# Kernel optimization log

Measured on AMD Instinct MI355X. Metric: run time of the kernel, lower is better.

## Reference

```python
import jax, jax.numpy as jnp
import numpy as np

T, B, F_IN = 1024, 256, 87


def _lstm(x, Wih, Whh, b):
    """PyTorch-convention LSTM over seq-first x [T,B,In]; gate order i,f,g,o."""
    H = Whh.shape[1]
    Bz = x.shape[1]

    def step(carry, xt):
        h, c = carry
        z = xt @ Wih.T + h @ Whh.T + b  # [B, 4H]
        i, f, g, o = jnp.split(z, 4, axis=-1)
        c = jax.nn.sigmoid(f) * c + jax.nn.sigmoid(i) * jnp.tanh(g)
        h = jax.nn.sigmoid(o) * jnp.tanh(c)
        return (h, c), h

    init = (jnp.zeros((Bz, H), x.dtype), jnp.zeros((Bz, H), x.dtype))
    _, ys = jax.lax.scan(step, init, x)
    return ys  # [T, B, H]


def setup_inputs() -> dict:
    key = jax.random.key(0)
    ks = jax.random.split(key, 24)

    def p(k, shape, fan):
        s = 1.0 / np.sqrt(fan)
        return jax.random.uniform(k, shape, jnp.float32, -s, s)

    d = {}
    d["x"] = jax.random.normal(ks[0], (T, B, F_IN), jnp.float32)
    # LSTM params (bias = b_ih + b_hh combined; forward-equivalent)
    dims = [(F_IN, 256), (256, 128), (128, 64), (64, 32)]
    ki = 1
    for li, (din, h) in enumerate(dims, start=1):
        d[f"w{li}i"] = p(ks[ki], (4 * h, din), h); ki += 1
        d[f"w{li}h"] = p(ks[ki], (4 * h, h), h); ki += 1
        d[f"b{li}"] = p(ks[ki], (4 * h,), h); ki += 1
    fcs = [(32, 128), (128, 64), (64, 32), (32, 3)]
    for fi, (din, dout) in enumerate(fcs, start=1):
        d[f"f{fi}w"] = p(ks[ki], (dout, din), din); ki += 1
        d[f"f{fi}b"] = p(ks[ki], (dout,), din); ki += 1
    return d


def reference(x, w1i, w1h, b1, w2i, w2h, b2, w3i, w3h, b3, w4i, w4h, b4,
              f1w, f1b, f2w, f2b, f3w, f3b, f4w, f4b):
    h = jnp.tanh(_lstm(x, w1i, w1h, b1))
    h = jnp.tanh(_lstm(h, w2i, w2h, b2))
    h = jnp.tanh(_lstm(h, w3i, w3h, b3))
    h = jnp.tanh(_lstm(h, w4i, w4h, b4)[0])  # [0] -> first timestep, [B,32]
    h = jax.nn.relu(h @ f1w.T + f1b)
    h = jax.nn.relu(h @ f2w.T + f2b)
    h = jax.nn.relu(h @ f3w.T + f3b)
    return h @ f4w.T + f4b  # [B, 3]
```

## Files before the change

### kernel.cpp

```cpp
#include <hip/hip_runtime.h>
#include <math.h>


#define O_W1T 0
#define O_W2T 66816
#define O_W3T 165120
#define O_W4T 189696
#define O_F1T 195840
#define O_F2T 199936
#define O_F3T 208128
#define O_B1  210176
#define O_B2  210944
#define O_B3  211328
#define O_B4  211520

__global__ __launch_bounds__(256) void prep_kernel(
    const float* __restrict__ w1i, const float* __restrict__ w2i,
    const float* __restrict__ w3i, const float* __restrict__ w4i,
    const float* __restrict__ b1,  const float* __restrict__ b2,
    const float* __restrict__ b3,  const float* __restrict__ b4,
    const float* __restrict__ f1w, const float* __restrict__ f2w,
    const float* __restrict__ f3w, float* __restrict__ ws)
{
    int i = blockIdx.x * 256 + threadIdx.x;
    if (i < 89088) {
        int row = i / 87, k = i - row * 87;
        int g = row >> 8;
        if (g != 1) {
            int base = (g == 0) ? 0 : (g == 2) ? 256 : 512;
            ws[O_W1T + k * 768 + base + (row & 255)] = w1i[i];
        }
    } else if (i < 220160) {
        int l = i - 89088;
        int row = l >> 8, k = l & 255;
        int g = row >> 7;
        if (g != 1) {
            int base = (g == 0) ? 0 : (g == 2) ? 128 : 256;
            ws[O_W2T + k * 384 + base + (row & 127)] = w2i[l];
        }
    } else if (i < 252928) {
        int l = i - 220160;
        int row = l >> 7, k = l & 127;
        int g = row >> 6;
        if (g != 1) {
            int base = (g == 0) ? 0 : (g == 2) ? 64 : 128;
            ws[O_W3T + k * 192 + base + (row & 63)] = w3i[l];
        }
    } else if (i < 261120) {
        int l = i - 252928;
        int row = l >> 6, k = l & 63;
        int g = row >> 5;
        if (g != 1) {
            int base = (g == 0) ? 0 : (g == 2) ? 32 : 64;
            ws[O_W4T + k * 96 + base + (row & 31)] = w4i[l];
        }
    } else if (i < 262144) {
        int l = i - 261120;
        int g = l >> 8;
        if (g != 1) {
            int base = (g == 0) ? 0 : (g == 2) ? 256 : 512;
            ws[O_B1 + base + (l & 255)] = b1[l];
        }
    } else if (i < 262656) {
        int l = i - 262144;
        int g = l >> 7;
        if (g != 1) {
            int base = (g == 0) ? 0 : (g == 2) ? 128 : 256;
            ws[O_B2 + base + (l & 127)] = b2[l];
        }
    } else if (i < 262912) {
        int l = i - 262656;
        int g = l >> 6;
        if (g != 1) {
            int base = (g == 0) ? 0 : (g == 2) ? 64 : 128;
            ws[O_B3 + base + (l & 63)] = b3[l];
        }
    } else if (i < 263040) {
        int l = i - 262912;
        int g = l >> 5;
        if (g != 1) {
            int base = (g == 0) ? 0 : (g == 2) ? 32 : 64;
            ws[O_B4 + base + (l & 31)] = b4[l];
        }
    } else if (i < 267136) {
        int l = i - 263040;
        int j = l >> 5, k = l & 31;
        ws[O_F1T + k * 128 + j] = f1w[l];
    } else if (i < 275328) {
        int l = i - 267136;
        int j = l >> 7, k = l & 127;
        ws[O_F2T + k * 64 + j] = f2w[l];
    } else if (i < 277376) {
        int l = i - 275328;
        int j = l >> 6, k = l & 63;
        ws[O_F3T + k * 32 + j] = f3w[l];
    }
}

__device__ __forceinline__ float frcp(float x) { return __builtin_amdgcn_rcpf(x); }
__device__ __forceinline__ float sigm(float x) { return frcp(1.0f + __expf(-x)); }
__device__ __forceinline__ float tanh_f(float x) { return 1.0f - 2.0f * frcp(1.0f + __expf(2.0f * x)); }
__device__ __forceinline__ float cell(float zi, float zg, float zo) {
    float c = sigm(zi) * tanh_f(zg);
    return tanh_f(sigm(zo) * tanh_f(c));
}

__global__ __launch_bounds__(256) void lstm_fused(
    const float* __restrict__ x, const float* __restrict__ ws,
    const float* __restrict__ f1b, const float* __restrict__ f2b,
    const float* __restrict__ f3b, const float* __restrict__ f4w,
    const float* __restrict__ f4b, float* __restrict__ out)
{
    const int t = threadIdx.x;
    const int r0 = blockIdx.x * 4;

    __shared__ __align__(16) float xsT[87][4];
    __shared__ __align__(16) float h1T[256][4];
    __shared__ __align__(16) float h2T[128][4];
    __shared__ __align__(16) float h3T[64][4];
    __shared__ __align__(16) float h4T[32][4];
    __shared__ __align__(16) float a1T[128][4];
    __shared__ __align__(16) float a2T[64][4];
    __shared__ __align__(16) float a3T[32][4];

    const float* W1T = ws + O_W1T;
    const float* W2T = ws + O_W2T;
    const float* W3T = ws + O_W3T;
    const float* W4T = ws + O_W4T;
    const float* F1T = ws + O_F1T;
    const float* F2T = ws + O_F2T;
    const float* F3T = ws + O_F3T;
    const float* B1p = ws + O_B1;
    const float* B2p = ws + O_B2;
    const float* B3p = ws + O_B3;
    const float* B4p = ws + O_B4;

    for (int idx = t; idx < 348; idx += 256) {
        int r = idx & 3, k = idx >> 2;
        xsT[k][r] = x[(r0 + r) * 87 + k];
    }
    __syncthreads();

    {
        float zi0, zi1, zi2, zi3, zg0, zg1, zg2, zg3, zo0, zo1, zo2, zo3;
        const float bi = B1p[t], bg = B1p[256 + t], bo = B1p[512 + t];
        zi0 = zi1 = zi2 = zi3 = bi;
        zg0 = zg1 = zg2 = zg3 = bg;
        zo0 = zo1 = zo2 = zo3 = bo;
        const float* w1 = W1T + t;
        #pragma unroll 8
        for (int k = 0; k < 87; ++k) {
            const float wi = w1[k * 768];
            const float wg = w1[k * 768 + 256];
            const float wo = w1[k * 768 + 512];
            const float4 xv = *(const float4*)(xsT[k]);
            zi0 = fmaf(xv.x, wi, zi0); zi1 = fmaf(xv.y, wi, zi1);
            zi2 = fmaf(xv.z, wi, zi2); zi3 = fmaf(xv.w, wi, zi3);
            zg0 = fmaf(xv.x, wg, zg0); zg1 = fmaf(xv.y, wg, zg1);
            zg2 = fmaf(xv.z, wg, zg2); zg3 = fmaf(xv.w, wg, zg3);
            zo0 = fmaf(xv.x, wo, zo0); zo1 = fmaf(xv.y, wo, zo1);
            zo2 = fmaf(xv.z, wo, zo2); zo3 = fmaf(xv.w, wo, zo3);
        }
        float4 hv;
        hv.x = cell(zi0, zg0, zo0);
        hv.y = cell(zi1, zg1, zo1);
        hv.z = cell(zi2, zg2, zo2);
        hv.w = cell(zi3, zg3, zo3);
        *(float4*)(h1T[t]) = hv;
    }
    __syncthreads();

    {
        const int j = t & 127, half = t >> 7;
        float zi0, zi1, zg0, zg1, zo0, zo1;
        zi0 = zi1 = B2p[j];
        zg0 = zg1 = B2p[128 + j];
        zo0 = zo1 = B2p[256 + j];
        const float* w2 = W2T + j;
        const float* hp = &h1T[0][half * 2];
        #pragma unroll 16
        for (int k = 0; k < 256; ++k) {
            const float wi = w2[k * 384];
            const float wg = w2[k * 384 + 128];
            const float wo = w2[k * 384 + 256];
            const float2 hv = *(const float2*)(hp + k * 4);
            zi0 = fmaf(hv.x, wi, zi0); zi1 = fmaf(hv.y, wi, zi1);
            zg0 = fmaf(hv.x, wg, zg0); zg1 = fmaf(hv.y, wg, zg1);
            zo0 = fmaf(hv.x, wo, zo0); zo1 = fmaf(hv.y, wo, zo1);
        }
        float2 r;
        r.x = cell(zi0, zg0, zo0);
        r.y = cell(zi1, zg1, zo1);
        *(float2*)(&h2T[j][half * 2]) = r;
    }
    __syncthreads();

    {
        const int j = t & 63, r = t >> 6;
        float zi = B3p[j], zg = B3p[64 + j], zo = B3p[128 + j];
        const float* w3 = W3T + j;
        #pragma unroll 16
        for (int k = 0; k < 128; ++k) {
            const float hv = h2T[k][r];
            zi = fmaf(hv, w3[k * 192], zi);
            zg = fmaf(hv, w3[k * 192 + 64], zg);
            zo = fmaf(hv, w3[k * 192 + 128], zo);
        }
        h3T[j][r] = cell(zi, zg, zo);
    }
    __syncthreads();

    if (t < 128) {
        const int j = t & 31, r = t >> 5;
        float zi = B4p[j], zg = B4p[32 + j], zo = B4p[64 + j];
        const float* w4 = W4T + j;
        #pragma unroll 16
        for (int k = 0; k < 64; ++k) {
            const float hv = h3T[k][r];
            zi = fmaf(hv, w4[k * 96], zi);
            zg = fmaf(hv, w4[k * 96 + 32], zg);
            zo = fmaf(hv, w4[k * 96 + 64], zo);
        }
        h4T[j][r] = cell(zi, zg, zo);
    }
    __syncthreads();

    {
        const int j = t & 127, half = t >> 7;
        float a0 = f1b[j], a1v = f1b[j];
        #pragma unroll
        for (int k = 0; k < 32; ++k) {
            const float w = F1T[k * 128 + j];
            const float2 hv = *(const float2*)(&h4T[k][half * 2]);
            a0  = fmaf(hv.x, w, a0);
            a1v = fmaf(hv.y, w, a1v);
        }
        float2 r;
        r.x = fmaxf(a0, 0.0f);
        r.y = fmaxf(a1v, 0.0f);
        *(float2*)(&a1T[j][half * 2]) = r;
    }
    __syncthreads();

    {
        const int j = t & 63, r = t >> 6;
        float a = f2b[j];
        #pragma unroll 16
        for (int k = 0; k < 128; ++k)
            a = fmaf(a1T[k][r], F2T[k * 64 + j], a);
        a2T[j][r] = fmaxf(a, 0.0f);
    }
    __syncthreads();

    if (t < 128) {
        const int j = t & 31, r = t >> 5;
        float a = f3b[j];
        #pragma unroll 16
        for (int k = 0; k < 64; ++k)
            a = fmaf(a2T[k][r], F3T[k * 32 + j], a);
        a3T[j][r] = fmaxf(a, 0.0f);
    }
    __syncthreads();

    if (t < 16) {
        const int r = t >> 2, o = t & 3;
        if (o < 3) {
            float a = f4b[o];
            #pragma unroll
            for (int k = 0; k < 32; ++k)
                a = fmaf(a3T[k][r], f4w[o * 32 + k], a);
            out[(r0 + r) * 3 + o] = a;
        }
    }
}

extern "C" void kernel_launch(void* const* d_in, const int* in_sizes, int n_in,
                              void* d_out, int out_size, void* d_ws, size_t ws_size,
                              hipStream_t stream) {
    const float* x   = (const float*)d_in[0];
    const float* w1i = (const float*)d_in[1];
    const float* b1  = (const float*)d_in[3];
    const float* w2i = (const float*)d_in[4];
    const float* b2  = (const float*)d_in[6];
    const float* w3i = (const float*)d_in[7];
    const float* b3  = (const float*)d_in[9];
    const float* w4i = (const float*)d_in[10];
    const float* b4  = (const float*)d_in[12];
    const float* f1w = (const float*)d_in[13];
    const float* f1b = (const float*)d_in[14];
    const float* f2w = (const float*)d_in[15];
    const float* f2b = (const float*)d_in[16];
    const float* f3w = (const float*)d_in[17];
    const float* f3b = (const float*)d_in[18];
    const float* f4w = (const float*)d_in[19];
    const float* f4b = (const float*)d_in[20];
    float* ws  = (float*)d_ws;
    float* out = (float*)d_out;

    prep_kernel<<<1084, 256, 0, stream>>>(w1i, w2i, w3i, w4i, b1, b2, b3, b4,
                                          f1w, f2w, f3w, ws);
    lstm_fused<<<64, 256, 0, stream>>>(x, ws, f1b, f2b, f3b, f4w, f4b, out);
}
```

Measured before the change: 183.6 us.

## Process one batch row per block with split-K partial sums across threads

The fused kernel now gives each block a single batch row instead of four and launches 256 blocks instead of 64, so more of the GPU's compute units have work. Inner layers split the reduction dimension across thread groups, write partial sums to shared memory, then reduce them, so all 256 threads stay busy on the narrower layers. In exchange, each weight element is fetched once per row rather than once per four rows, which adds L2 traffic, and each layer now needs extra barriers.

```diff
diff --git a/kernel.cpp b/kernel.cpp
--- a/kernel.cpp
+++ b/kernel.cpp
@@ -112,16 +112,12 @@
     const float* __restrict__ f4b, float* __restrict__ out)
 {
     const int t = threadIdx.x;
-    const int r0 = blockIdx.x * 4;
-
-    __shared__ __align__(16) float xsT[87][4];
-    __shared__ __align__(16) float h1T[256][4];
-    __shared__ __align__(16) float h2T[128][4];
-    __shared__ __align__(16) float h3T[64][4];
-    __shared__ __align__(16) float h4T[32][4];
-    __shared__ __align__(16) float a1T[128][4];
-    __shared__ __align__(16) float a2T[64][4];
-    __shared__ __align__(16) float a3T[32][4];
+    const int r = blockIdx.x;
+
+    __shared__ float xs[87];
+    __shared__ float h1[256], h2[128], h3[64], h4[32];
+    __shared__ float a1[128], a2[64], a3[32];
+    __shared__ float ps[768];
 
     const float* W1T = ws + O_W1T;
     const float* W2T = ws + O_W2T;
@@ -135,142 +131,162 @@
     const float* B3p = ws + O_B3;
     const float* B4p = ws + O_B4;
 
-    for (int idx = t; idx < 348; idx += 256) {
-        int r = idx & 3, k = idx >> 2;
-        xsT[k][r] = x[(r0 + r) * 87 + k];
-    }
-    __syncthreads();
-
-    {
-        float zi0, zi1, zi2, zi3, zg0, zg1, zg2, zg3, zo0, zo1, zo2, zo3;
-        const float bi = B1p[t], bg = B1p[256 + t], bo = B1p[512 + t];
-        zi0 = zi1 = zi2 = zi3 = bi;
-        zg0 = zg1 = zg2 = zg3 = bg;
-        zo0 = zo1 = zo2 = zo3 = bo;
-        const float* w1 = W1T + t;
+    if (t < 87) xs[t] = x[r * 87 + t];
+    __syncthreads();
+
+    {
+        float zi = B1p[t], zg = B1p[256 + t], zo = B1p[512 + t];
+        const float* w = W1T + t;
         #pragma unroll 8
         for (int k = 0; k < 87; ++k) {
-            const float wi = w1[k * 768];
-            const float wg = w1[k * 768 + 256];
-            const float wo = w1[k * 768 + 512];
-            const float4 xv = *(const float4*)(xsT[k]);
-            zi0 = fmaf(xv.x, wi, zi0); zi1 = fmaf(xv.y, wi, zi1);
-            zi2 = fmaf(xv.z, wi, zi2); zi3 = fmaf(xv.w, wi, zi3);
-            zg0 = fmaf(xv.x, wg, zg0); zg1 = fmaf(xv.y, wg, zg1);
-            zg2 = fmaf(xv.z, wg, zg2); zg3 = fmaf(xv.w, wg, zg3);
-            zo0 = fmaf(xv.x, wo, zo0); zo1 = fmaf(xv.y, wo, zo1);
-            zo2 = fmaf(xv.z, wo, zo2); zo3 = fmaf(xv.w, wo, zo3);
-        }
-        float4 hv;
-        hv.x = cell(zi0, zg0, zo0);
-        hv.y = cell(zi1, zg1, zo1);
-        hv.z = cell(zi2, zg2, zo2);
-        hv.w = cell(zi3, zg3, zo3);
-        *(float4*)(h1T[t]) = hv;
-    }
-    __syncthreads();
-
-    {
-        const int j = t & 127, half = t >> 7;
-        float zi0, zi1, zg0, zg1, zo0, zo1;
-        zi0 = zi1 = B2p[j];
-        zg0 = zg1 = B2p[128 + j];
-        zo0 = zo1 = B2p[256 + j];
-        const float* w2 = W2T + j;
-        const float* hp = &h1T[0][half * 2];
-        #pragma unroll 16
-        for (int k = 0; k < 256; ++k) {
-            const float wi = w2[k * 384];
-            const float wg = w2[k * 384 + 128];
-            const float wo = w2[k * 384 + 256];
-            const float2 hv = *(const float2*)(hp + k * 4);
-            zi0 = fmaf(hv.x, wi, zi0); zi1 = fmaf(hv.y, wi, zi1);
-            zg0 = fmaf(hv.x, wg, zg0); zg1 = fmaf(hv.y, wg, zg1);
-            zo0 = fmaf(hv.x, wo, zo0); zo1 = fmaf(hv.y, wo, zo1);
-        }
-        float2 r;
-        r.x = cell(zi0, zg0, zo0);
-        r.y = cell(zi1, zg1, zo1);
-        *(float2*)(&h2T[j][half * 2]) = r;
-    }
-    __syncthreads();
-
-    {
-        const int j = t & 63, r = t >> 6;
-        float zi = B3p[j], zg = B3p[64 + j], zo = B3p[128 + j];
-        const float* w3 = W3T + j;
-        #pragma unroll 16
-        for (int k = 0; k < 128; ++k) {
-            const float hv = h2T[k][r];
-            zi = fmaf(hv, w3[k * 192], zi);
-            zg = fmaf(hv, w3[k * 192 + 64], zg);
-            zo = fmaf(hv, w3[k * 192 + 128], zo);
-        }
-        h3T[j][r] = cell(zi, zg, zo);
-    }
-    __syncthreads();
-
-    if (t < 128) {
-        const int j = t & 31, r = t >> 5;
-        float zi = B4p[j], zg = B4p[32 + j], zo = B4p[64 + j];
-        const float* w4 = W4T + j;
-        #pragma unroll 16
-        for (int k = 0; k < 64; ++k) {
-            const float hv = h3T[k][r];
-            zi = fmaf(hv, w4[k * 96], zi);
-            zg = fmaf(hv, w4[k * 96 + 32], zg);
-            zo = fmaf(hv, w4[k * 96 + 64], zo);
-        }
-        h4T[j][r] = cell(zi, zg, zo);
-    }
-    __syncthreads();
-
-    {
-        const int j = t & 127, half = t >> 7;
-        float a0 = f1b[j], a1v = f1b[j];
-        #pragma unroll
-        for (int k = 0; k < 32; ++k) {
-            const float w = F1T[k * 128 + j];
-            const float2 hv = *(const float2*)(&h4T[k][half * 2]);
-            a0  = fmaf(hv.x, w, a0);
-            a1v = fmaf(hv.y, w, a1v);
-        }
-        float2 r;
-        r.x = fmaxf(a0, 0.0f);
-        r.y = fmaxf(a1v, 0.0f);
-        *(float2*)(&a1T[j][half * 2]) = r;
-    }
-    __syncthreads();
-
-    {
-        const int j = t & 63, r = t >> 6;
-        float a = f2b[j];
-        #pragma unroll 16
-        for (int k = 0; k < 128; ++k)
-            a = fmaf(a1T[k][r], F2T[k * 64 + j], a);
-        a2T[j][r] = fmaxf(a, 0.0f);
-    }
-    __syncthreads();
-
-    if (t < 128) {
-        const int j = t & 31, r = t >> 5;
-        float a = f3b[j];
-        #pragma unroll 16
-        for (int k = 0; k < 64; ++k)
-            a = fmaf(a2T[k][r], F3T[k * 32 + j], a);
-        a3T[j][r] = fmaxf(a, 0.0f);
-    }
-    __syncthreads();
-
-    if (t < 16) {
-        const int r = t >> 2, o = t & 3;
-        if (o < 3) {
-            float a = f4b[o];
-            #pragma unroll
-            for (int k = 0; k < 32; ++k)
-                a = fmaf(a3T[k][r], f4w[o * 32 + k], a);
-            out[(r0 + r) * 3 + o] = a;
-        }
+            const float xv = xs[k];
+            zi = fmaf(xv, w[k * 768],       zi);
+            zg = fmaf(xv, w[k * 768 + 256], zg);
+            zo = fmaf(xv, w[k * 768 + 512], zo);
+        }
+        h1[t] = cell(zi, zg, zo);
+    }
+    __syncthreads();
+
+    {
+        const int j = t & 127, q = t >> 7;
+        float zi = q ? 0.0f : B2p[j];
+        float zg = q ? 0.0f : B2p[128 + j];
+        float zo = q ? 0.0f : B2p[256 + j];
+        const float* w = W2T + j;
+        const int k0 = q * 128;
+        #pragma unroll 8
+        for (int k = k0; k < k0 + 128; ++k) {
+            const float hv = h1[k];
+            zi = fmaf(hv, w[k * 384],       zi);
+            zg = fmaf(hv, w[k * 384 + 128], zg);
+            zo = fmaf(hv, w[k * 384 + 256], zo);
+        }
+        ps[q * 384 + j]       = zi;
+        ps[q * 384 + 128 + j] = zg;
+        ps[q * 384 + 256 + j] = zo;
+    }
+    __syncthreads();
+    if (t < 128)
+        h2[t] = cell(ps[t] + ps[384 + t],
+                     ps[128 + t] + ps[512 + t],
+                     ps[256 + t] + ps[640 + t]);
+    __syncthreads();
+
+    {
+        const int j = t & 63, q = t >> 6;
+        float zi = q ? 0.0f : B3p[j];
+        float zg = q ? 0.0f : B3p[64 + j];
+        float zo = q ? 0.0f : B3p[128 + j];
+        const float* w = W3T + j;
+        const int k0 = q * 32;
+        #pragma unroll 8
+        for (int k = k0; k < k0 + 32; ++k) {
+            const float hv = h2[k];
+            zi = fmaf(hv, w[k * 192],       zi);
+            zg = fmaf(hv, w[k * 192 + 64],  zg);
+            zo = fmaf(hv, w[k * 192 + 128], zo);
+        }
+        ps[q * 192 + j]       = zi;
+        ps[q * 192 + 64 + j]  = zg;
+        ps[q * 192 + 128 + j] = zo;
+    }
+    __syncthreads();
+    if (t < 64) {
+        float zi = 0.0f, zg = 0.0f, zo = 0.0f;
+        #pragma unroll
+        for (int q = 0; q < 4; ++q) {
+            zi += ps[q * 192 + t];
+            zg += ps[q * 192 + 64 + t];
+            zo += ps[q * 192 + 128 + t];
+        }
+        h3[t] = cell(zi, zg, zo);
+    }
+    __syncthreads();
+
+    {
+        const int j = t & 31, q = t >> 5;
+        float zi = (q == 0) ? B4p[j] : 0.0f;
+        float zg = (q == 0) ? B4p[32 + j] : 0.0f;
+        float zo = (q == 0) ? B4p[64 + j] : 0.0f;
+        const float* w = W4T + j;
+        const int k0 = q * 8;
+        #pragma unroll
+        for (int k = k0; k < k0 + 8; ++k) {
+            const float hv = h3[k];
+            zi = fmaf(hv, w[k * 96],      zi);
+            zg = fmaf(hv, w[k * 96 + 32], zg);
+            zo = fmaf(hv, w[k * 96 + 64], zo);
+        }
+        ps[q * 96 + j]      = zi;
+        ps[q * 96 + 32 + j] = zg;
+        ps[q * 96 + 64 + j] = zo;
+    }
+    __syncthreads();
+    if (t < 32) {
+        float zi = 0.0f, zg = 0.0f, zo = 0.0f;
+        #pragma unroll
+        for (int q = 0; q < 8; ++q) {
+            zi += ps[q * 96 + t];
+            zg += ps[q * 96 + 32 + t];
+            zo += ps[q * 96 + 64 + t];
+        }
+        h4[t] = cell(zi, zg, zo);
+    }
+    __syncthreads();
+
+    {
+        const int j = t & 127, q = t >> 7;
+        float a = q ? 0.0f : f1b[j];
+        const int k0 = q * 16;
+        #pragma unroll
+        for (int k = k0; k < k0 + 16; ++k)
+            a = fmaf(h4[k], F1T[k * 128 + j], a);
+        ps[q * 128 + j] = a;
+    }
+    __syncthreads();
+    if (t < 128) a1[t] = fmaxf(ps[t] + ps[128 + t], 0.0f);
+    __syncthreads();
+
+    {
+        const int j = t & 63, q = t >> 6;
+        float a = q ? 0.0f : f2b[j];
+        const int k0 = q * 32;
+        #pragma unroll 8
+        for (int k = k0; k < k0 + 32; ++k)
+            a = fmaf(a1[k], F2T[k * 64 + j], a);
+        ps[q * 64 + j] = a;
+    }
+    __syncthreads();
+    if (t < 64)
+        a2[t] = fmaxf(ps[t] + ps[64 + t] + ps[128 + t] + ps[192 + t], 0.0f);
+    __syncthreads();
+
+    {
+        const int j = t & 31, q = t >> 5;
+        float a = (q == 0) ? f3b[j] : 0.0f;
+        const int k0 = q * 8;
+        #pragma unroll
+        for (int k = k0; k < k0 + 8; ++k)
+            a = fmaf(a2[k], F3T[k * 32 + j], a);
+        ps[q * 32 + j] = a;
+    }
+    __syncthreads();
+    if (t < 32) {
+        float a = 0.0f;
+        #pragma unroll
+        for (int q = 0; q < 8; ++q) a += ps[q * 32 + t];
+        a3[t] = fmaxf(a, 0.0f);
+    }
+    __syncthreads();
+
+    if (t < 3) {
+        float a = f4b[t];
+        const float* w = f4w + t * 32;
+        #pragma unroll 8
+        for (int k = 0; k < 32; ++k)
+            a = fmaf(a3[k], w[k], a);
+        out[r * 3 + t] = a;
     }
 }
 
@@ -299,5 +315,5 @@
 
     prep_kernel<<<1084, 256, 0, stream>>>(w1i, w2i, w3i, w4i, b1, b2, b3, b4,
                                           f1w, f2w, f3w, ws);
-    lstm_fused<<<64, 256, 0, stream>>>(x, ws, f1b, f2b, f3b, f4w, f4b, out);
+    lstm_fused<<<256, 256, 0, stream>>>(x, ws, f1b, f2b, f3b, f4w, f4b, out);
 }
```

Measured after the change: 173.2 us. 5.7% less time.
